# Kernel tuning notes

Hardware: AMD Instinct MI355X
Metric: run time of the kernel (lower is better)

The kernel has to match this reference:

```python
import jax, jax.numpy as jnp
import numpy as np
import math

EMBED_DIM = 256
NUM_HEADS = 8
HEAD_DIM = EMBED_DIM // NUM_HEADS


def rope(t):
    # t: (B, h, S, d). Standard rotate-half RoPE over sequence positions.
    B, h, S, d = t.shape
    half = d // 2
    inv_freq = 1.0 / (10000.0 ** (jnp.arange(0, half, dtype=jnp.float32) / half))
    ang = jnp.arange(S, dtype=jnp.float32)[:, None] * inv_freq[None, :]  # (S, d/2)
    cos = jnp.concatenate([jnp.cos(ang), jnp.cos(ang)], axis=-1)  # (S, d)
    sin = jnp.concatenate([jnp.sin(ang), jnp.sin(ang)], axis=-1)
    t1, t2 = t[..., :half], t[..., half:]
    rot = jnp.concatenate([-t2, t1], axis=-1)
    return t * cos + rot * sin


def setup_inputs() -> dict:
    key = jax.random.key(0)
    ks = jax.random.split(key, 8)
    B, H, W, C = 2, 64, 48, EMBED_DIM
    s = 1.0 / math.sqrt(C)
    return {
        "x": jax.random.normal(ks[0], (B, H, W, C), dtype=jnp.float32),
        "Wq": jax.random.normal(ks[1], (C, C), dtype=jnp.float32) * s,
        "Wk": jax.random.normal(ks[2], (C, C), dtype=jnp.float32) * s,
        "Wv": jax.random.normal(ks[3], (C, C), dtype=jnp.float32) * s,
        "q_bias": jnp.zeros((C,), dtype=jnp.float32),
        "v_bias": jnp.zeros((C,), dtype=jnp.float32),
        "Wo": jax.random.normal(ks[4], (C, C), dtype=jnp.float32) * s,
        "bo": jnp.zeros((C,), dtype=jnp.float32),
    }


def reference(x, Wq, Wk, Wv, q_bias, v_bias, Wo, bo):
    B, H, W, C = x.shape
    S = H * W
    h, d = NUM_HEADS, HEAD_DIM
    xf = x.reshape(B, S, C)
    # QKV projections (torch F.linear: y = x @ W.T + b)
    q = xf @ Wq.T + q_bias
    k = xf @ Wk.T
    v = xf @ Wv.T + v_bias
    # (B, S, h, d) -> (B, h, S, d)
    q = q.reshape(B, S, h, d).transpose(0, 2, 1, 3)
    k = k.reshape(B, S, h, d).transpose(0, 2, 1, 3)
    v = v.reshape(B, S, h, d).transpose(0, 2, 1, 3)
    q = rope(q)
    k = rope(k)
    scale = 1.0 / math.sqrt(d)
    scores = jnp.einsum('bhsd,bhtd->bhst', q, k) * scale  # (B, h, S, S)
    attn = jax.nn.softmax(scores, axis=-1)
    ctx = jnp.einsum('bhst,bhtd->bhsd', attn, v)  # (B, h, S, d)
    ctx = ctx.transpose(0, 2, 1, 3).reshape(B, S, C)
    return ctx @ Wo.T + bo
```

## Files before the change

### kernel.cpp

```cpp
#include <hip/hip_runtime.h>
#include <math.h>

#define B_   2
#define S_   3072
#define C_   256
#define NH   8
#define HD   32
#define HALF 16
#define NELEM (B_*S_*C_)
#define MLROWS (B_*NH*S_)
#define TABN  (S_*HALF)

typedef __attribute__((ext_vector_type(8))) __bf16 bf16x8;
typedef __attribute__((ext_vector_type(4))) float  f32x4;

__device__ __forceinline__ float dot4(float4 a, float4 b) {
    return a.x*b.x + a.y*b.y + a.z*b.z + a.w*b.w;
}

__device__ __forceinline__ void gload_lds16(const void* g, void* l) {
    __builtin_amdgcn_global_load_lds(
        (const __attribute__((address_space(1))) unsigned int*)g,
        (__attribute__((address_space(3))) unsigned int*)l, 16, 0, 0);
}

__device__ __forceinline__ void bsplit(float x, unsigned short& h, unsigned short& lo) {
    __bf16 hb = (__bf16)x;
    float hf = (float)hb;
    __bf16 lb = (__bf16)(x - hf);
    h  = __builtin_bit_cast(unsigned short, hb);
    lo = __builtin_bit_cast(unsigned short, lb);
}

__global__ __launch_bounds__(256) void fsplit_kernel(const float* __restrict__ src,
        unsigned short* __restrict__ hi, unsigned short* __restrict__ lo)
{
    const size_t i = (size_t)blockIdx.x * 256 + threadIdx.x;
    float4 xv = *(const float4*)&src[i*4];
    ushort4 h, l; unsigned short hh, ll;
    bsplit(xv.x, hh, ll); h.x = hh; l.x = ll;
    bsplit(xv.y, hh, ll); h.y = hh; l.y = ll;
    bsplit(xv.z, hh, ll); h.z = hh; l.z = ll;
    bsplit(xv.w, hh, ll); h.w = hh; l.w = ll;
    *(ushort4*)&hi[i*4] = h;
    *(ushort4*)&lo[i*4] = l;
}

__global__ __launch_bounds__(256) void wsplit_kernel(
        const float* __restrict__ Wq, const float* __restrict__ Wk,
        const float* __restrict__ Wv, const float* __restrict__ Wo,
        unsigned short* __restrict__ wqh, unsigned short* __restrict__ wql,
        unsigned short* __restrict__ wkh, unsigned short* __restrict__ wkl,
        unsigned short* __restrict__ wvh, unsigned short* __restrict__ wvl,
        unsigned short* __restrict__ woh, unsigned short* __restrict__ wol)
{
    const float* src; unsigned short *h, *l;
    if      (blockIdx.y == 0) { src = Wq; h = wqh; l = wql; }
    else if (blockIdx.y == 1) { src = Wk; h = wkh; l = wkl; }
    else if (blockIdx.y == 2) { src = Wv; h = wvh; l = wvl; }
    else                      { src = Wo; h = woh; l = wol; }
    const size_t i = (size_t)blockIdx.x * 256 + threadIdx.x;
    float4 xv = *(const float4*)&src[i*4];
    ushort4 hv, lv; unsigned short hh, ll;
    bsplit(xv.x, hh, ll); hv.x = hh; lv.x = ll;
    bsplit(xv.y, hh, ll); hv.y = hh; lv.y = ll;
    bsplit(xv.z, hh, ll); hv.z = hh; lv.z = ll;
    bsplit(xv.w, hh, ll); hv.w = hh; lv.w = ll;
    *(ushort4*)&h[i*4] = hv;
    *(ushort4*)&l[i*4] = lv;
}

__device__ __forceinline__ void gemm_mfma_body(
        const unsigned short* __restrict__ Ahi, const unsigned short* __restrict__ Alo,
        const unsigned short* __restrict__ Whi, const unsigned short* __restrict__ Wlo,
        const float* __restrict__ bias, float* __restrict__ out, float scl)
{
    const int tid = threadIdx.x;
    const int cq  = tid & 15;
    const int gq  = tid >> 4;
    const int m0  = blockIdx.x * 32;
    const int n0  = blockIdx.y * 32;

    const size_t a0 = (size_t)(m0 + cq)      * C_ + gq*8;
    const size_t a1 = (size_t)(m0 + 16 + cq) * C_ + gq*8;
    const size_t w0 = (size_t)(n0 + cq)      * C_ + gq*8;
    const size_t w1 = (size_t)(n0 + 16 + cq) * C_ + gq*8;

    f32x4 acc00 = {0,0,0,0}, acc01 = {0,0,0,0};
    f32x4 acc10 = {0,0,0,0}, acc11 = {0,0,0,0};

    #pragma unroll
    for (int kk = 0; kk < 8; ++kk) {
        const int ko = kk * 32;
        const bf16x8 wh0 = *(const bf16x8*)(Whi + w0 + ko);
        const bf16x8 wh1 = *(const bf16x8*)(Whi + w1 + ko);
        const bf16x8 wl0 = *(const bf16x8*)(Wlo + w0 + ko);
        const bf16x8 wl1 = *(const bf16x8*)(Wlo + w1 + ko);
        const bf16x8 ah0 = *(const bf16x8*)(Ahi + a0 + ko);
        const bf16x8 ah1 = *(const bf16x8*)(Ahi + a1 + ko);
        const bf16x8 al0 = *(const bf16x8*)(Alo + a0 + ko);
        const bf16x8 al1 = *(const bf16x8*)(Alo + a1 + ko);
        acc00 = __builtin_amdgcn_mfma_f32_16x16x32_bf16(wh0, ah0, acc00, 0, 0, 0);
        acc01 = __builtin_amdgcn_mfma_f32_16x16x32_bf16(wh0, ah1, acc01, 0, 0, 0);
        acc10 = __builtin_amdgcn_mfma_f32_16x16x32_bf16(wh1, ah0, acc10, 0, 0, 0);
        acc11 = __builtin_amdgcn_mfma_f32_16x16x32_bf16(wh1, ah1, acc11, 0, 0, 0);
        acc00 = __builtin_amdgcn_mfma_f32_16x16x32_bf16(wh0, al0, acc00, 0, 0, 0);
        acc01 = __builtin_amdgcn_mfma_f32_16x16x32_bf16(wh0, al1, acc01, 0, 0, 0);
        acc10 = __builtin_amdgcn_mfma_f32_16x16x32_bf16(wh1, al0, acc10, 0, 0, 0);
        acc11 = __builtin_amdgcn_mfma_f32_16x16x32_bf16(wh1, al1, acc11, 0, 0, 0);
        acc00 = __builtin_amdgcn_mfma_f32_16x16x32_bf16(wl0, ah0, acc00, 0, 0, 0);
        acc01 = __builtin_amdgcn_mfma_f32_16x16x32_bf16(wl0, ah1, acc01, 0, 0, 0);
        acc10 = __builtin_amdgcn_mfma_f32_16x16x32_bf16(wl1, ah0, acc10, 0, 0, 0);
        acc11 = __builtin_amdgcn_mfma_f32_16x16x32_bf16(wl1, ah1, acc11, 0, 0, 0);
    }

    float4 bv0 = make_float4(0.f, 0.f, 0.f, 0.f);
    float4 bv1 = make_float4(0.f, 0.f, 0.f, 0.f);
    if (bias) {
        bv0 = *(const float4*)&bias[n0 + 4*gq];
        bv1 = *(const float4*)&bias[n0 + 16 + 4*gq];
    }
    float4 o;
    o = make_float4((acc00[0]+bv0.x)*scl, (acc00[1]+bv0.y)*scl,
                    (acc00[2]+bv0.z)*scl, (acc00[3]+bv0.w)*scl);
    *(float4*)&out[(size_t)(m0 + cq)*C_ + n0 + 4*gq] = o;
    o = make_float4((acc01[0]+bv0.x)*scl, (acc01[1]+bv0.y)*scl,
                    (acc01[2]+bv0.z)*scl, (acc01[3]+bv0.w)*scl);
    *(float4*)&out[(size_t)(m0 + 16 + cq)*C_ + n0 + 4*gq] = o;
    o = make_float4((acc10[0]+bv1.x)*scl, (acc10[1]+bv1.y)*scl,
                    (acc10[2]+bv1.z)*scl, (acc10[3]+bv1.w)*scl);
    *(float4*)&out[(size_t)(m0 + cq)*C_ + n0 + 16 + 4*gq] = o;
    o = make_float4((acc11[0]+bv1.x)*scl, (acc11[1]+bv1.y)*scl,
                    (acc11[2]+bv1.z)*scl, (acc11[3]+bv1.w)*scl);
    *(float4*)&out[(size_t)(m0 + 16 + cq)*C_ + n0 + 16 + 4*gq] = o;
}

__global__ __launch_bounds__(64) void qkv_mfma_kernel(
        const unsigned short* __restrict__ xhi, const unsigned short* __restrict__ xlo,
        const unsigned short* __restrict__ wqh, const unsigned short* __restrict__ wql,
        const unsigned short* __restrict__ wkh, const unsigned short* __restrict__ wkl,
        const unsigned short* __restrict__ wvh, const unsigned short* __restrict__ wvl,
        const float* __restrict__ qb, const float* __restrict__ vb,
        float* __restrict__ q, float* __restrict__ k, float* __restrict__ v)
{
    if (blockIdx.z == 0)
        gemm_mfma_body(xhi, xlo, wqh, wql, qb, q, 0.17677669529663687f);
    else if (blockIdx.z == 1)
        gemm_mfma_body(xhi, xlo, wkh, wkl, nullptr, k, 1.0f);
    else
        gemm_mfma_body(xhi, xlo, wvh, wvl, vb, v, 1.0f);
}

__global__ __launch_bounds__(64) void out_gemm_mfma_kernel(
        const unsigned short* __restrict__ chi, const unsigned short* __restrict__ clo,
        const unsigned short* __restrict__ woh, const unsigned short* __restrict__ wol,
        const float* __restrict__ bo, float* __restrict__ out)
{
    gemm_mfma_body(chi, clo, woh, wol, bo, out, 1.0f);
}

__device__ __forceinline__ void gemm_nt_body(const float* __restrict__ A,
                                             const float* __restrict__ W,
                                             const float* __restrict__ bias,
                                             float* __restrict__ out,
                                             float scl)
{
    __shared__ float As[2][64*32];
    __shared__ float Ws[2][64*32];

    const int tid  = threadIdx.x;
    const int wv   = tid >> 6;
    const int tx4  = (tid & 15) * 4;
    const int ty4  = (tid >> 4) * 4;
    const int row0 = blockIdx.x * 64;
    const int col0 = blockIdx.y * 64;

    const int d0  = tid, d1 = tid + 256;
    const int r0s = d0 >> 3, r1s = d1 >> 3;
    const int c0s = (d0 & 7) ^ ((r0s >> 2) & 7);
    const int c1s = (d1 & 7) ^ ((r1s >> 2) & 7);
    const float* a0p = A + (size_t)(row0 + r0s)*C_ + c0s*4;
    const float* a1p = A + (size_t)(row0 + r1s)*C_ + c1s*4;
    const float* w0p = W + (size_t)(col0 + r0s)*C_ + c0s*4;
    const float* w1p = W + (size_t)(col0 + r1s)*C_ + c1s*4;
    const int dst = wv * 256;

#define GSTAGE(kc, buf) { \
        gload_lds16(a0p + (kc), &As[buf][dst]);        \
        gload_lds16(a1p + (kc), &As[buf][dst + 1024]); \
        gload_lds16(w0p + (kc), &Ws[buf][dst]);        \
        gload_lds16(w1p + (kc), &Ws[buf][dst + 1024]); }

    float acc[4][4] = {};
    const int xa = ((tid >> 4) & 7) * 4;
    const int xw = (tid & 7) * 4;

    GSTAGE(0, 0);
    __syncthreads();

    for (int kk = 0; kk < 8; ++kk) {
        const int buf = kk & 1;
        if (kk + 1 < 8) GSTAGE((kk + 1) * 32, buf ^ 1);

        const float* Ab = &As[buf][ty4 * 32];
        const float* Wb = &Ws[buf][tx4 * 32];
        #pragma unroll
        for (int p = 0; p < 8; ++p) {
            const int oa = (p * 4) ^ xa;
            const int ow = (p * 4) ^ xw;
            float4 a0 = *(const float4*)&Ab[oa];
            float4 a1 = *(const float4*)&Ab[32 + oa];
            float4 a2 = *(const float4*)&Ab[64 + oa];
            float4 a3 = *(const float4*)&Ab[96 + oa];
            float4 w0 = *(const float4*)&Wb[ow];
            float4 w1 = *(const float4*)&Wb[32 + ow];
            float4 w2 = *(const float4*)&Wb[64 + ow];
            float4 w3 = *(const float4*)&Wb[96 + ow];
            acc[0][0] += dot4(a0,w0); acc[0][1] += dot4(a0,w1);
            acc[0][2] += dot4(a0,w2); acc[0][3] += dot4(a0,w3);
            acc[1][0] += dot4(a1,w0); acc[1][1] += dot4(a1,w1);
            acc[1][2] += dot4(a1,w2); acc[1][3] += dot4(a1,w3);
            acc[2][0] += dot4(a2,w0); acc[2][1] += dot4(a2,w1);
            acc[2][2] += dot4(a2,w2); acc[2][3] += dot4(a2,w3);
            acc[3][0] += dot4(a3,w0); acc[3][1] += dot4(a3,w1);
            acc[3][2] += dot4(a3,w2); acc[3][3] += dot4(a3,w3);
        }
        __syncthreads();
    }
#undef GSTAGE

    float4 bv = make_float4(0.f, 0.f, 0.f, 0.f);
    if (bias) bv = *(const float4*)&bias[col0 + tx4];
    #pragma unroll
    for (int rr = 0; rr < 4; ++rr) {
        float4 o = make_float4((acc[rr][0] + bv.x)*scl, (acc[rr][1] + bv.y)*scl,
                               (acc[rr][2] + bv.z)*scl, (acc[rr][3] + bv.w)*scl);
        *(float4*)&out[(size_t)(row0 + ty4 + rr)*C_ + col0 + tx4] = o;
    }
}

__global__ __launch_bounds__(256) void qkv_kernel(
        const float* __restrict__ x,
        const float* __restrict__ Wq, const float* __restrict__ Wk, const float* __restrict__ Wv,
        const float* __restrict__ qb, const float* __restrict__ vb,
        float* __restrict__ q, float* __restrict__ k, float* __restrict__ v)
{
    if      (blockIdx.z == 0) gemm_nt_body(x, Wq, qb,      q, 0.17677669529663687f);
    else if (blockIdx.z == 1) gemm_nt_body(x, Wk, nullptr, k, 1.0f);
    else                      gemm_nt_body(x, Wv, vb,      v, 1.0f);
}

__global__ __launch_bounds__(256) void out_gemm_kernel(
        const float* __restrict__ ctx, const float* __restrict__ Wo,
        const float* __restrict__ bo, float* __restrict__ out)
{
    gemm_nt_body(ctx, Wo, bo, out, 1.0f);
}

__global__ __launch_bounds__(256) void rope_tab_kernel(float2* __restrict__ tbl)
{
    const int idx = blockIdx.x * 256 + threadIdx.x;
    const int j = idx & 15;
    const int s = idx >> 4;
    const double invf = exp(-log(10000.0) * (double)j * (1.0 / 16.0));
    const float  angf = (float)((double)s * invf);
    double sn, cs;
    sincos((double)angf, &sn, &cs);
    tbl[idx] = make_float2((float)cs, (float)sn);
}

template<bool TAB>
__global__ __launch_bounds__(256) void rope_kernel(float* __restrict__ q, float* __restrict__ k,
                                                   const float2* __restrict__ tbl,
                                                   unsigned short* __restrict__ qhi,
                                                   unsigned short* __restrict__ qlo,
                                                   unsigned short* __restrict__ khi,
                                                   unsigned short* __restrict__ klo)
{
    const int idx = blockIdx.x * 256 + threadIdx.x;
    const int per_tensor = B_ * S_ * NH * HALF;
    const bool isq = (idx < per_tensor);
    float* t = isq ? q : k;
    const int i   = isq ? idx : idx - per_tensor;
    const int j   = i & 15;
    const int hh  = (i >> 4) & 7;
    const int row = i >> 7;
    const int s   = (row >= S_) ? (row - S_) : row;

    float c, sf;
    if (TAB) {
        const float2 cs2 = tbl[(s << 4) | j];
        c = cs2.x; sf = cs2.y;
    } else {
        const double invf = exp(-log(10000.0) * (double)j * (1.0 / 16.0));
        const float  angf = (float)((double)s * invf);
        double sn, cd;
        sincos((double)angf, &sn, &cd);
        c = (float)cd; sf = (float)sn;
    }

    const size_t base = (size_t)row * C_ + hh * HD + j;
    const float t1 = t[base];
    const float t2 = t[base + HALF];
    const float o1 = t1 * c - t2 * sf;
    const float o2 = t2 * c + t1 * sf;
    t[base]        = o1;
    t[base + HALF] = o2;

    if (TAB) {
        unsigned short* hi = isq ? qhi : khi;
        unsigned short* lo = isq ? qlo : klo;
        const size_t sb = ((size_t)row * NH + hh) * 32;
        unsigned short h1, l1, h2, l2;
        bsplit(o1, h1, l1);
        bsplit(o2, h2, l2);
        hi[sb + j]      = h1;  lo[sb + j]      = l1;
        hi[sb + j + 16] = h2;  lo[sb + j + 16] = l2;
    }
}

__global__ __launch_bounds__(256) void vsplit_kernel(const float* __restrict__ v,
                                                     unsigned short* __restrict__ vthi,
                                                     unsigned short* __restrict__ vtlo)
{
    __shared__ float T[64][33];
    const int t  = threadIdx.x;
    const int kb = blockIdx.x;
    const int hh = blockIdx.y;
    const int b  = blockIdx.z;
    const size_t rowbase = (size_t)b*S_ + kb*64;

    {
        const int r = t >> 2;
        const int p = t & 3;
        float4 a  = *(const float4*)&v[(rowbase + r)*C_ + hh*32 + p*4];
        float4 b2 = *(const float4*)&v[(rowbase + r)*C_ + hh*32 + 16 + p*4];
        *(float4*)&T[r][p*4]      = a;
        *(float4*)&T[r][16 + p*4] = b2;
    }
    __syncthreads();

    const int d = t >> 3;
    const int j = t & 7;
    const int pa = (j & 1)*16 + ((j & 2) ? 4 : 0);
    const int pb = pa + 8;
    ushort4 ha, la, hb, lb;
    unsigned short hs, ls;
    {
        float x0 = T[8*j+0][d], x1 = T[8*j+1][d], x2 = T[8*j+2][d], x3 = T[8*j+3][d];
        bsplit(x0, hs, ls); ha.x = hs; la.x = ls;
        bsplit(x1, hs, ls); ha.y = hs; la.y = ls;
        bsplit(x2, hs, ls); ha.z = hs; la.z = ls;
        bsplit(x3, hs, ls); ha.w = hs; la.w = ls;
        float y0 = T[8*j+4][d], y1 = T[8*j+5][d], y2 = T[8*j+6][d], y3 = T[8*j+7][d];
        bsplit(y0, hs, ls); hb.x = hs; lb.x = ls;
        bsplit(y1, hs, ls); hb.y = hs; lb.y = ls;
        bsplit(y2, hs, ls); hb.z = hs; lb.z = ls;
        bsplit(y3, hs, ls); hb.w = hs; lb.w = ls;
    }
    const size_t ob = (((size_t)b*NH + hh)*32 + d)*S_ + (size_t)(kb*2 + (j >> 2))*32;
    *(ushort4*)&vthi[ob + pa] = ha;
    *(ushort4*)&vthi[ob + pb] = hb;
    *(ushort4*)&vtlo[ob + pa] = la;
    *(ushort4*)&vtlo[ob + pb] = lb;
}

template<int NSPLIT>
__global__ __launch_bounds__(64) void attn_mfma(
        const unsigned short* __restrict__ qhi, const unsigned short* __restrict__ qlo,
        const unsigned short* __restrict__ khi, const unsigned short* __restrict__ klo,
        const unsigned short* __restrict__ vthi, const unsigned short* __restrict__ vtlo,
        float* __restrict__ outp, float* __restrict__ pm, float* __restrict__ pl)
{
    __shared__ unsigned short KH[1024];
    __shared__ unsigned short KL[1024];
    __shared__ unsigned short VTH[2][1024];
    __shared__ unsigned short VTL[2][1024];

    const int tid = threadIdx.x;
    const int cq  = tid & 15;
    const int gq  = tid >> 4;
    const int qb  = blockIdx.x * 32;
    const int hh  = blockIdx.y;
    const int split = blockIdx.z % NSPLIT;
    const int b     = blockIdx.z / NSPLIT;
    const int kt0   = split * (S_ / NSPLIT);
    const int NT    = (S_ / NSPLIT) / 32;

    const size_t rowbase = (size_t)b * S_;
    const int coloff = hh * HD;

    const int sd = tid >> 2;
    const int sp = tid & 3;
    const int ss = sp ^ ((sd >> 1) & 3);

    const unsigned short* kh0 = khi + ((rowbase + kt0 + sd)*NH + hh)*32 + ss*8;
    const unsigned short* kl0 = klo + ((rowbase + kt0 + sd)*NH + hh)*32 + ss*8;
    const size_t vrow_a = (((size_t)b*NH + hh)*32 + sd)      * S_ + kt0;
    const size_t vrow_b = (((size_t)b*NH + hh)*32 + sd + 16) * S_ + kt0;
    const unsigned short* vh_a = vthi + vrow_a + ss*8;
    const unsigned short* vh_b = vthi + vrow_b + ss*8;
    const unsigned short* vl_a = vtlo + vrow_a + ss*8;
    const unsigned short* vl_b = vtlo + vrow_b + ss*8;

#define ISSUE_TILE(t_, vb_) { \
        const size_t ko = (size_t)(t_)*(32*NH*32); \
        const size_t vo = (size_t)(t_)*32; \
        gload_lds16(kh0 + ko,            &KH[0]);   \
        gload_lds16(kh0 + ko + 16*NH*32, &KH[512]); \
        gload_lds16(kl0 + ko,            &KL[0]);   \
        gload_lds16(kl0 + ko + 16*NH*32, &KL[512]); \
        gload_lds16(vh_a + vo, &VTH[vb_][0]);   \
        gload_lds16(vh_b + vo, &VTH[vb_][512]); \
        gload_lds16(vl_a + vo, &VTL[vb_][0]);   \
        gload_lds16(vl_b + vo, &VTL[vb_][512]); }

    ISSUE_TILE(0, 0);

    const size_t q0off = ((rowbase + qb +      cq)*NH + hh)*32 + gq*8;
    const size_t q1off = ((rowbase + qb + 16 + cq)*NH + hh)*32 + gq*8;
    const bf16x8 q0h = *(const bf16x8*)(qhi + q0off);
    const bf16x8 q0l = *(const bf16x8*)(qlo + q0off);
    const bf16x8 q1h = *(const bf16x8*)(qhi + q1off);
    const bf16x8 q1l = *(const bf16x8*)(qlo + q1off);

    const int slot = gq ^ ((cq >> 1) & 3);
    const int fo   = cq*32 + slot*8;

    float m = -1e30f;
    float l0 = 0.f, l1 = 0.f;
    f32x4 acc00 = {0,0,0,0}, acc01 = {0,0,0,0};
    f32x4 acc10 = {0,0,0,0}, acc11 = {0,0,0,0};

    for (int t = 0; t < NT; ++t) {
        const int cur = t & 1;
        asm volatile("s_waitcnt vmcnt(0)" ::: "memory");
        __builtin_amdgcn_sched_barrier(0);

        const bf16x8 kh0f = *(const bf16x8*)&KH[fo];
        const bf16x8 kh1f = *(const bf16x8*)&KH[512 + fo];
        const bf16x8 kl0f = *(const bf16x8*)&KL[fo];
        const bf16x8 kl1f = *(const bf16x8*)&KL[512 + fo];
        asm volatile("s_waitcnt lgkmcnt(0)" ::: "memory");
        __builtin_amdgcn_sched_barrier(0);
        if (t + 1 < NT) ISSUE_TILE(t + 1, cur ^ 1);

        __builtin_amdgcn_s_setprio(1);
        f32x4 s00 = {0,0,0,0}, s01 = {0,0,0,0}, s10 = {0,0,0,0}, s11 = {0,0,0,0};
        s00 = __builtin_amdgcn_mfma_f32_16x16x32_bf16(kh0f, q0h, s00, 0, 0, 0);
        s01 = __builtin_amdgcn_mfma_f32_16x16x32_bf16(kh1f, q0h, s01, 0, 0, 0);
        s10 = __builtin_amdgcn_mfma_f32_16x16x32_bf16(kh0f, q1h, s10, 0, 0, 0);
        s11 = __builtin_amdgcn_mfma_f32_16x16x32_bf16(kh1f, q1h, s11, 0, 0, 0);
        s00 = __builtin_amdgcn_mfma_f32_16x16x32_bf16(kh0f, q0l, s00, 0, 0, 0);
        s01 = __builtin_amdgcn_mfma_f32_16x16x32_bf16(kh1f, q0l, s01, 0, 0, 0);
        s10 = __builtin_amdgcn_mfma_f32_16x16x32_bf16(kh0f, q1l, s10, 0, 0, 0);
        s11 = __builtin_amdgcn_mfma_f32_16x16x32_bf16(kh1f, q1l, s11, 0, 0, 0);
        s00 = __builtin_amdgcn_mfma_f32_16x16x32_bf16(kl0f, q0h, s00, 0, 0, 0);
        s01 = __builtin_amdgcn_mfma_f32_16x16x32_bf16(kl1f, q0h, s01, 0, 0, 0);
        s10 = __builtin_amdgcn_mfma_f32_16x16x32_bf16(kl0f, q1h, s10, 0, 0, 0);
        s11 = __builtin_amdgcn_mfma_f32_16x16x32_bf16(kl1f, q1h, s11, 0, 0, 0);

        float lmax;
        {
            float a = fmaxf(fmaxf(s00[0], s00[1]), fmaxf(s00[2], s00[3]));
            float b2 = fmaxf(fmaxf(s01[0], s01[1]), fmaxf(s01[2], s01[3]));
            float c2 = fmaxf(fmaxf(s10[0], s10[1]), fmaxf(s10[2], s10[3]));
            float d2 = fmaxf(fmaxf(s11[0], s11[1]), fmaxf(s11[2], s11[3]));
            lmax = fmaxf(fmaxf(a, b2), fmaxf(c2, d2));
        }
        if (!__all(lmax - m <= 8.f)) {
            float wm = lmax;
            wm = fmaxf(wm, __shfl_xor(wm, 1));  wm = fmaxf(wm, __shfl_xor(wm, 2));
            wm = fmaxf(wm, __shfl_xor(wm, 4));  wm = fmaxf(wm, __shfl_xor(wm, 8));
            wm = fmaxf(wm, __shfl_xor(wm, 16)); wm = fmaxf(wm, __shfl_xor(wm, 32));
            const float mn = fmaxf(m, wm);
            const float f = __expf(m - mn);
            m = mn; l0 *= f; l1 *= f;
            #pragma unroll
            for (int e = 0; e < 4; ++e) {
                acc00[e] *= f; acc01[e] *= f; acc10[e] *= f; acc11[e] *= f;
            }
        }
        float p00[4], p01[4], p10[4], p11[4];
        #pragma unroll
        for (int e = 0; e < 4; ++e) {
            p00[e] = __expf(s00[e] - m);
            p01[e] = __expf(s01[e] - m);
            p10[e] = __expf(s10[e] - m);
            p11[e] = __expf(s11[e] - m);
        }
        l0 += ((p00[0]+p00[1]) + (p00[2]+p00[3])) + ((p01[0]+p01[1]) + (p01[2]+p01[3]));
        l1 += ((p10[0]+p10[1]) + (p10[2]+p10[3])) + ((p11[0]+p11[1]) + (p11[2]+p11[3]));

        bf16x8 pah0, pal0, pah1, pal1;
        #pragma unroll
        for (int e = 0; e < 4; ++e) {
            __bf16 h;
            h = (__bf16)p00[e]; pah0[e]   = h; pal0[e]   = (__bf16)(p00[e] - (float)h);
            h = (__bf16)p01[e]; pah0[e+4] = h; pal0[e+4] = (__bf16)(p01[e] - (float)h);
            h = (__bf16)p10[e]; pah1[e]   = h; pal1[e]   = (__bf16)(p10[e] - (float)h);
            h = (__bf16)p11[e]; pah1[e+4] = h; pal1[e+4] = (__bf16)(p11[e] - (float)h);
        }

        const bf16x8 vh0 = *(const bf16x8*)&VTH[cur][fo];
        const bf16x8 vh1 = *(const bf16x8*)&VTH[cur][512 + fo];
        const bf16x8 vl0 = *(const bf16x8*)&VTL[cur][fo];
        const bf16x8 vl1 = *(const bf16x8*)&VTL[cur][512 + fo];

        acc00 = __builtin_amdgcn_mfma_f32_16x16x32_bf16(pah0, vh0, acc00, 0, 0, 0);
        acc01 = __builtin_amdgcn_mfma_f32_16x16x32_bf16(pah0, vh1, acc01, 0, 0, 0);
        acc10 = __builtin_amdgcn_mfma_f32_16x16x32_bf16(pah1, vh0, acc10, 0, 0, 0);
        acc11 = __builtin_amdgcn_mfma_f32_16x16x32_bf16(pah1, vh1, acc11, 0, 0, 0);
        acc00 = __builtin_amdgcn_mfma_f32_16x16x32_bf16(pah0, vl0, acc00, 0, 0, 0);
        acc01 = __builtin_amdgcn_mfma_f32_16x16x32_bf16(pah0, vl1, acc01, 0, 0, 0);
        acc10 = __builtin_amdgcn_mfma_f32_16x16x32_bf16(pah1, vl0, acc10, 0, 0, 0);
        acc11 = __builtin_amdgcn_mfma_f32_16x16x32_bf16(pah1, vl1, acc11, 0, 0, 0);
        acc00 = __builtin_amdgcn_mfma_f32_16x16x32_bf16(pal0, vh0, acc00, 0, 0, 0);
        acc01 = __builtin_amdgcn_mfma_f32_16x16x32_bf16(pal0, vh1, acc01, 0, 0, 0);
        acc10 = __builtin_amdgcn_mfma_f32_16x16x32_bf16(pal1, vh0, acc10, 0, 0, 0);
        acc11 = __builtin_amdgcn_mfma_f32_16x16x32_bf16(pal1, vh1, acc11, 0, 0, 0);
        __builtin_amdgcn_s_setprio(0);
    }
#undef ISSUE_TILE

    l0 += __shfl_xor(l0, 16); l0 += __shfl_xor(l0, 32);
    l1 += __shfl_xor(l1, 16); l1 += __shfl_xor(l1, 32);

    float lq0[4], lq1[4];
    #pragma unroll
    for (int r = 0; r < 4; ++r) {
        lq0[r] = __shfl(l0, 4*gq + r);
        lq1[r] = __shfl(l1, 4*gq + r);
    }

    float* obase = (NSPLIT == 1) ? outp : (outp + (size_t)split * NELEM);
    #pragma unroll
    for (int r = 0; r < 4; ++r) {
        const int qrow = qb + 4*gq + r;
        const float i0 = (NSPLIT == 1) ? 1.f / lq0[r] : 1.f;
        const float i1 = (NSPLIT == 1) ? 1.f / lq1[r] : 1.f;
        obase[(rowbase + qrow)*C_ + coloff + cq]           = acc00[r]*i0;
        obase[(rowbase + qrow)*C_ + coloff + 16 + cq]      = acc01[r]*i0;
        obase[(rowbase + qrow + 16)*C_ + coloff + cq]      = acc10[r]*i1;
        obase[(rowbase + qrow + 16)*C_ + coloff + 16 + cq] = acc11[r]*i1;
    }

    if (NSPLIT > 1 && gq == 0) {
        const size_t mlb = (size_t)split*MLROWS + ((size_t)b*NH + hh)*S_;
        pm[mlb + qb + cq]      = m;  pl[mlb + qb + cq]      = l0;
        pm[mlb + qb + 16 + cq] = m;  pl[mlb + qb + 16 + cq] = l1;
    }
}

__global__ __launch_bounds__(64) void attn_fp32(
        const float* __restrict__ q, const float* __restrict__ k,
        const float* __restrict__ v, float* __restrict__ outp)
{
    __shared__ float SM[2][2][16*32];

    const int tid  = threadIdx.x;
    const int sub  = tid & 3;
    const int g    = tid >> 2;
    const int qb   = blockIdx.x * 32;
    const int hh   = blockIdx.y;
    const int b    = blockIdx.z;
    const int NT   = S_ / 16;

    const size_t rowbase = (size_t)b * S_;
    const int coloff = hh * HD;

    const int srow  = tid >> 3;
    const int sxcol = (((tid & 7) ^ (srow & 3)) << 2);
    const float* kstage = &k[(rowbase + srow)*C_ + coloff + sxcol];
    const float* vstage = &v[(rowbase + srow)*C_ + coloff + sxcol];

    const int r0 = qb + g, r1 = qb + g + 16;

#define ISSUE_TILE(t_, bufi) { \
        const float* gk = kstage + (size_t)(t_)*(16*C_); \
        const float* gv = vstage + (size_t)(t_)*(16*C_); \
        float* lk = &SM[bufi][0][0]; \
        float* lv = &SM[bufi][1][0]; \
        gload_lds16(gk        , lk      ); \
        gload_lds16(gk +  8*C_, lk + 256); \
        gload_lds16(gv        , lv      ); \
        gload_lds16(gv +  8*C_, lv + 256); }

    ISSUE_TILE(0, 0);

    float q0[32], q1[32];
    #pragma unroll
    for (int k4 = 0; k4 < 32; k4 += 4) {
        float4 t0 = *(const float4*)&q[(rowbase + r0)*C_ + coloff + k4];
        float4 t1 = *(const float4*)&q[(rowbase + r1)*C_ + coloff + k4];
        q0[k4+0]=t0.x; q0[k4+1]=t0.y; q0[k4+2]=t0.z; q0[k4+3]=t0.w;
        q1[k4+0]=t1.x; q1[k4+1]=t1.y; q1[k4+2]=t1.z; q1[k4+3]=t1.w;
    }

    float m0 = -1e30f, m1 = -1e30f, l0 = 0.f, l1 = 0.f;
    float a0[32] = {}, a1[32] = {};

    for (int t = 0; t < NT; ++t) {
        const int cur = t & 1;
        if (t + 1 < NT) {
            ISSUE_TILE(t + 1, cur ^ 1);
            asm volatile("s_waitcnt vmcnt(4)" ::: "memory");
        } else {
            asm volatile("s_waitcnt vmcnt(0)" ::: "memory");
        }
        __builtin_amdgcn_sched_barrier(0);

        const float* Kc = &SM[cur][0][0];
        const float* Vc = &SM[cur][1][0];

        float s0_[4], s1_[4];
        #pragma unroll
        for (int i = 0; i < 4; ++i) {
            const float* kr = Kc + (sub + 4*i)*32;
            float d0 = 0.f, d1 = 0.f;
            #pragma unroll
            for (int c4 = 0; c4 < 8; ++c4) {
                float4 kk = *(const float4*)&kr[(c4 ^ sub) << 2];
                d0 += q0[c4*4+0]*kk.x + q0[c4*4+1]*kk.y + q0[c4*4+2]*kk.z + q0[c4*4+3]*kk.w;
                d1 += q1[c4*4+0]*kk.x + q1[c4*4+1]*kk.y + q1[c4*4+2]*kk.z + q1[c4*4+3]*kk.w;
            }
            s0_[i] = d0; s1_[i] = d1;
        }
        {
            float tm0 = fmaxf(fmaxf(s0_[0], s0_[1]), fmaxf(s0_[2], s0_[3]));
            float tm1 = fmaxf(fmaxf(s1_[0], s1_[1]), fmaxf(s1_[2], s1_[3]));
            tm0 = fmaxf(tm0, __shfl_xor(tm0, 1)); tm0 = fmaxf(tm0, __shfl_xor(tm0, 2));
            tm1 = fmaxf(tm1, __shfl_xor(tm1, 1)); tm1 = fmaxf(tm1, __shfl_xor(tm1, 2));
            if (!__all((tm0 - m0 <= 8.f) && (tm1 - m1 <= 8.f))) {
                const float mn0 = fmaxf(m0, tm0), mn1 = fmaxf(m1, tm1);
                const float f0 = __expf(m0 - mn0), f1 = __expf(m1 - mn1);
                m0 = mn0; m1 = mn1; l0 *= f0; l1 *= f1;
                #pragma unroll
                for (int d = 0; d < 32; ++d) { a0[d] *= f0; a1[d] *= f1; }
            }
            #pragma unroll
            for (int i = 0; i < 4; ++i) {
                s0_[i] = __expf(s0_[i] - m0);
                s1_[i] = __expf(s1_[i] - m1);
            }
            l0 += (s0_[0] + s0_[1]) + (s0_[2] + s0_[3]);
            l1 += (s1_[0] + s1_[1]) + (s1_[2] + s1_[3]);
        }
        #pragma unroll
        for (int i = 0; i < 4; ++i) {
            const float* vr = Vc + (sub + 4*i)*32;
            const float pj0 = s0_[i], pj1 = s1_[i];
            #pragma unroll
            for (int d4 = 0; d4 < 8; ++d4) {
                float4 vv = *(const float4*)&vr[(d4 ^ sub) << 2];
                a0[d4*4+0] += pj0*vv.x; a0[d4*4+1] += pj0*vv.y;
                a0[d4*4+2] += pj0*vv.z; a0[d4*4+3] += pj0*vv.w;
                a1[d4*4+0] += pj1*vv.x; a1[d4*4+1] += pj1*vv.y;
                a1[d4*4+2] += pj1*vv.z; a1[d4*4+3] += pj1*vv.w;
            }
        }
    }
#undef ISSUE_TILE

    l0 += __shfl_xor(l0, 1); l0 += __shfl_xor(l0, 2);
    l1 += __shfl_xor(l1, 1); l1 += __shfl_xor(l1, 2);
    const float inv0 = 1.f / l0, inv1 = 1.f / l1;
    #pragma unroll
    for (int d = 0; d < 32; ++d) {
        float x0 = a0[d]; x0 += __shfl_xor(x0, 1); x0 += __shfl_xor(x0, 2); a0[d] = x0 * inv0;
        float x1 = a1[d]; x1 += __shfl_xor(x1, 1); x1 += __shfl_xor(x1, 2); a1[d] = x1 * inv1;
    }
    #define WRITE_SLICE(ro, a_, off) { \
        float4 o1 = make_float4(a_[(off)+0],a_[(off)+1],a_[(off)+2],a_[(off)+3]); \
        float4 o2 = make_float4(a_[(off)+4],a_[(off)+5],a_[(off)+6],a_[(off)+7]); \
        *(float4*)&outp[(rowbase + (ro))*C_ + coloff + (off)]     = o1; \
        *(float4*)&outp[(rowbase + (ro))*C_ + coloff + (off) + 4] = o2; }
    if      (sub == 0) { WRITE_SLICE(r0, a0, 0)  WRITE_SLICE(r1, a1, 0)  }
    else if (sub == 1) { WRITE_SLICE(r0, a0, 8)  WRITE_SLICE(r1, a1, 8)  }
    else if (sub == 2) { WRITE_SLICE(r0, a0, 16) WRITE_SLICE(r1, a1, 16) }
    else               { WRITE_SLICE(r0, a0, 24) WRITE_SLICE(r1, a1, 24) }
    #undef WRITE_SLICE
}

template<int NSPLIT>
__global__ __launch_bounds__(256) void combine_split_kernel(
        const float* __restrict__ pacc, const float* __restrict__ pm,
        const float* __restrict__ pl,
        unsigned short* __restrict__ chi, unsigned short* __restrict__ clo)
{
    const int gid = blockIdx.x * 256 + threadIdx.x;
    int rem = gid >> 3;
    const int h = rem & 7; rem >>= 3;
    const int s = rem % S_;
    const int b = rem / S_;

    const size_t i0 = ((size_t)b*NH + h)*S_ + s;
    float mm[NSPLIT], ll[NSPLIT], w[NSPLIT];
    float M = -1e30f;
    #pragma unroll
    for (int i = 0; i < NSPLIT; ++i) {
        mm[i] = pm[i0 + (size_t)i*MLROWS];
        ll[i] = pl[i0 + (size_t)i*MLROWS];
        M = fmaxf(M, mm[i]);
    }
    float L = 0.f;
    #pragma unroll
    for (int i = 0; i < NSPLIT; ++i) { w[i] = __expf(mm[i] - M); L += ll[i]*w[i]; }
    const float invL = 1.f / L;

    const size_t a = (size_t)gid * 4;
    float4 o = make_float4(0.f, 0.f, 0.f, 0.f);
    #pragma unroll
    for (int i = 0; i < NSPLIT; ++i) {
        const float4 x = *(const float4*)&pacc[a + (size_t)i*NELEM];
        o.x += x.x*w[i]; o.y += x.y*w[i]; o.z += x.z*w[i]; o.w += x.w*w[i];
    }
    o.x *= invL; o.y *= invL; o.z *= invL; o.w *= invL;
    ushort4 hv, lv; unsigned short hh, ll2;
    bsplit(o.x, hh, ll2); hv.x = hh; lv.x = ll2;
    bsplit(o.y, hh, ll2); hv.y = hh; lv.y = ll2;
    bsplit(o.z, hh, ll2); hv.z = hh; lv.z = ll2;
    bsplit(o.w, hh, ll2); hv.w = hh; lv.w = ll2;
    *(ushort4*)&chi[a] = hv;
    *(ushort4*)&clo[a] = lv;
}

extern "C" void kernel_launch(void* const* d_in, const int* in_sizes, int n_in,
                              void* d_out, int out_size, void* d_ws, size_t ws_size,
                              hipStream_t stream)
{
    const float* x  = (const float*)d_in[0];
    const float* Wq = (const float*)d_in[1];
    const float* Wk = (const float*)d_in[2];
    const float* Wv = (const float*)d_in[3];
    const float* qb = (const float*)d_in[4];
    const float* vb = (const float*)d_in[5];
    const float* Wo = (const float*)d_in[6];
    const float* bo = (const float*)d_in[7];
    float* out = (float*)d_out;

    float* ws   = (float*)d_ws;
    float* q    = ws;
    float* k    = q + NELEM;
    float* v    = k + NELEM;
    float* ctx  = v + NELEM;
    float* tblf = ctx + NELEM;
    float* pacc = tblf + 2*TABN;
    float* pm   = pacc + (size_t)2*NELEM;
    float* pl   = pm + (size_t)2*MLROWS;
    unsigned short* qhi  = (unsigned short*)(pl + (size_t)2*MLROWS);
    unsigned short* qlo  = qhi + (size_t)NELEM;
    unsigned short* khi  = qlo + (size_t)NELEM;
    unsigned short* klo  = khi + (size_t)NELEM;
    unsigned short* vthi = klo + (size_t)NELEM;
    unsigned short* vtlo = vthi + (size_t)NELEM;

    unsigned short* xhi = (unsigned short*)pacc;
    unsigned short* xlo = xhi + (size_t)NELEM;
    unsigned short* wqh = xlo + (size_t)NELEM;
    unsigned short* wql = wqh + 65536;
    unsigned short* wkh = wql + 65536;
    unsigned short* wkl = wkh + 65536;
    unsigned short* wvh = wkl + 65536;
    unsigned short* wvl = wvh + 65536;
    unsigned short* woh = (unsigned short*)ctx;
    unsigned short* wol = woh + 65536;
    unsigned short* chi = qhi;
    unsigned short* clo = qlo;

    const size_t need = ((size_t)9*NELEM + 2*TABN + 4*MLROWS) * sizeof(float);

    if (ws_size >= need) {
        float2* tbl = (float2*)tblf;
        fsplit_kernel<<<NELEM/1024, 256, 0, stream>>>(x, xhi, xlo);
        wsplit_kernel<<<dim3(64, 4), 256, 0, stream>>>(Wq, Wk, Wv, Wo,
                wqh, wql, wkh, wkl, wvh, wvl, woh, wol);
        qkv_mfma_kernel<<<dim3((B_*S_)/32, C_/32, 3), 64, 0, stream>>>(
                xhi, xlo, wqh, wql, wkh, wkl, wvh, wvl, qb, vb, q, k, v);
        rope_tab_kernel<<<TABN/256, 256, 0, stream>>>(tbl);
        rope_kernel<true><<<6144, 256, 0, stream>>>(q, k, tbl, qhi, qlo, khi, klo);
        vsplit_kernel<<<dim3(S_/64, NH, B_), 256, 0, stream>>>(v, vthi, vtlo);
        attn_mfma<2><<<dim3(S_/32, NH, B_*2), 64, 0, stream>>>(
            qhi, qlo, khi, klo, vthi, vtlo, pacc, pm, pl);
        combine_split_kernel<2><<<(B_*S_*NH*8)/256, 256, 0, stream>>>(
            pacc, pm, pl, chi, clo);
        out_gemm_mfma_kernel<<<dim3((B_*S_)/32, C_/32), 64, 0, stream>>>(
            chi, clo, woh, wol, bo, out);
    } else {
        qkv_kernel<<<dim3(96, 4, 3), 256, 0, stream>>>(x, Wq, Wk, Wv, qb, vb, q, k, v);
        rope_kernel<false><<<6144, 256, 0, stream>>>(q, k, nullptr,
                                                     nullptr, nullptr, nullptr, nullptr);
        attn_fp32<<<dim3(S_/32, NH, B_), 64, 0, stream>>>(q, k, v, ctx);
        out_gemm_kernel<<<dim3(96, 4, 1), 256, 0, stream>>>(ctx, Wo, bo, out);
    }
}
```

Before: 172.8 us.

## Fuse prep kernels and load attention K/V tiles directly into registers

```diff
diff --git a/kernel.cpp b/kernel.cpp
--- a/kernel.cpp
+++ b/kernel.cpp
@@ -32,42 +32,56 @@
     lo = __builtin_bit_cast(unsigned short, lb);
 }
 
-__global__ __launch_bounds__(256) void fsplit_kernel(const float* __restrict__ src,
-        unsigned short* __restrict__ hi, unsigned short* __restrict__ lo)
-{
-    const size_t i = (size_t)blockIdx.x * 256 + threadIdx.x;
-    float4 xv = *(const float4*)&src[i*4];
-    ushort4 h, l; unsigned short hh, ll;
-    bsplit(xv.x, hh, ll); h.x = hh; l.x = ll;
-    bsplit(xv.y, hh, ll); h.y = hh; l.y = ll;
-    bsplit(xv.z, hh, ll); h.z = hh; l.z = ll;
-    bsplit(xv.w, hh, ll); h.w = hh; l.w = ll;
-    *(ushort4*)&hi[i*4] = h;
-    *(ushort4*)&lo[i*4] = l;
-}
-
-__global__ __launch_bounds__(256) void wsplit_kernel(
+__global__ __launch_bounds__(256) void prep_kernel(
+        const float* __restrict__ x,
         const float* __restrict__ Wq, const float* __restrict__ Wk,
         const float* __restrict__ Wv, const float* __restrict__ Wo,
+        unsigned short* __restrict__ xhi, unsigned short* __restrict__ xlo,
         unsigned short* __restrict__ wqh, unsigned short* __restrict__ wql,
         unsigned short* __restrict__ wkh, unsigned short* __restrict__ wkl,
         unsigned short* __restrict__ wvh, unsigned short* __restrict__ wvl,
-        unsigned short* __restrict__ woh, unsigned short* __restrict__ wol)
-{
-    const float* src; unsigned short *h, *l;
-    if      (blockIdx.y == 0) { src = Wq; h = wqh; l = wql; }
-    else if (blockIdx.y == 1) { src = Wk; h = wkh; l = wkl; }
-    else if (blockIdx.y == 2) { src = Wv; h = wvh; l = wvl; }
-    else                      { src = Wo; h = woh; l = wol; }
-    const size_t i = (size_t)blockIdx.x * 256 + threadIdx.x;
-    float4 xv = *(const float4*)&src[i*4];
-    ushort4 hv, lv; unsigned short hh, ll;
-    bsplit(xv.x, hh, ll); hv.x = hh; lv.x = ll;
-    bsplit(xv.y, hh, ll); hv.y = hh; lv.y = ll;
-    bsplit(xv.z, hh, ll); hv.z = hh; lv.z = ll;
-    bsplit(xv.w, hh, ll); hv.w = hh; lv.w = ll;
-    *(ushort4*)&h[i*4] = hv;
-    *(ushort4*)&l[i*4] = lv;
+        unsigned short* __restrict__ woh, unsigned short* __restrict__ wol,
+        float2* __restrict__ tbl)
+{
+    const int bx = blockIdx.x;
+    const int tid = threadIdx.x;
+    if (bx < 1536) {
+        const size_t i = (size_t)bx * 256 + tid;
+        float4 xv = *(const float4*)&x[i*4];
+        ushort4 h, l; unsigned short hh, ll;
+        bsplit(xv.x, hh, ll); h.x = hh; l.x = ll;
+        bsplit(xv.y, hh, ll); h.y = hh; l.y = ll;
+        bsplit(xv.z, hh, ll); h.z = hh; l.z = ll;
+        bsplit(xv.w, hh, ll); h.w = hh; l.w = ll;
+        *(ushort4*)&xhi[i*4] = h;
+        *(ushort4*)&xlo[i*4] = l;
+    } else if (bx < 1792) {
+        const int wb  = bx - 1536;
+        const int mat = wb >> 6;
+        const float* src; unsigned short *h, *l;
+        if      (mat == 0) { src = Wq; h = wqh; l = wql; }
+        else if (mat == 1) { src = Wk; h = wkh; l = wkl; }
+        else if (mat == 2) { src = Wv; h = wvh; l = wvl; }
+        else               { src = Wo; h = woh; l = wol; }
+        const size_t i = (size_t)(wb & 63) * 256 + tid;
+        float4 xv = *(const float4*)&src[i*4];
+        ushort4 hv, lv; unsigned short hh, ll;
+        bsplit(xv.x, hh, ll); hv.x = hh; lv.x = ll;
+        bsplit(xv.y, hh, ll); hv.y = hh; lv.y = ll;
+        bsplit(xv.z, hh, ll); hv.z = hh; lv.z = ll;
+        bsplit(xv.w, hh, ll); hv.w = hh; lv.w = ll;
+        *(ushort4*)&h[i*4] = hv;
+        *(ushort4*)&l[i*4] = lv;
+    } else {
+        const int idx = (bx - 1792) * 256 + tid;
+        const int j = idx & 15;
+        const int s = idx >> 4;
+        const double invf = exp(-log(10000.0) * (double)j * (1.0 / 16.0));
+        const float  angf = (float)((double)s * invf);
+        double sn, cs;
+        sincos((double)angf, &sn, &cs);
+        tbl[idx] = make_float2((float)cs, (float)sn);
+    }
 }
 
 __device__ __forceinline__ void gemm_mfma_body(
@@ -257,18 +271,6 @@
     gemm_nt_body(ctx, Wo, bo, out, 1.0f);
 }
 
-__global__ __launch_bounds__(256) void rope_tab_kernel(float2* __restrict__ tbl)
-{
-    const int idx = blockIdx.x * 256 + threadIdx.x;
-    const int j = idx & 15;
-    const int s = idx >> 4;
-    const double invf = exp(-log(10000.0) * (double)j * (1.0 / 16.0));
-    const float  angf = (float)((double)s * invf);
-    double sn, cs;
-    sincos((double)angf, &sn, &cs);
-    tbl[idx] = make_float2((float)cs, (float)sn);
-}
-
 template<bool TAB>
 __global__ __launch_bounds__(256) void rope_kernel(float* __restrict__ q, float* __restrict__ k,
                                                    const float2* __restrict__ tbl,
@@ -372,11 +374,6 @@
         const unsigned short* __restrict__ vthi, const unsigned short* __restrict__ vtlo,
         float* __restrict__ outp, float* __restrict__ pm, float* __restrict__ pl)
 {
-    __shared__ unsigned short KH[1024];
-    __shared__ unsigned short KL[1024];
-    __shared__ unsigned short VTH[2][1024];
-    __shared__ unsigned short VTL[2][1024];
-
     const int tid = threadIdx.x;
     const int cq  = tid & 15;
     const int gq  = tid >> 4;
@@ -390,32 +387,20 @@
     const size_t rowbase = (size_t)b * S_;
     const int coloff = hh * HD;
 
-    const int sd = tid >> 2;
-    const int sp = tid & 3;
-    const int ss = sp ^ ((sd >> 1) & 3);
-
-    const unsigned short* kh0 = khi + ((rowbase + kt0 + sd)*NH + hh)*32 + ss*8;
-    const unsigned short* kl0 = klo + ((rowbase + kt0 + sd)*NH + hh)*32 + ss*8;
-    const size_t vrow_a = (((size_t)b*NH + hh)*32 + sd)      * S_ + kt0;
-    const size_t vrow_b = (((size_t)b*NH + hh)*32 + sd + 16) * S_ + kt0;
-    const unsigned short* vh_a = vthi + vrow_a + ss*8;
-    const unsigned short* vh_b = vthi + vrow_b + ss*8;
-    const unsigned short* vl_a = vtlo + vrow_a + ss*8;
-    const unsigned short* vl_b = vtlo + vrow_b + ss*8;
-
-#define ISSUE_TILE(t_, vb_) { \
-        const size_t ko = (size_t)(t_)*(32*NH*32); \
-        const size_t vo = (size_t)(t_)*32; \
-        gload_lds16(kh0 + ko,            &KH[0]);   \
-        gload_lds16(kh0 + ko + 16*NH*32, &KH[512]); \
-        gload_lds16(kl0 + ko,            &KL[0]);   \
-        gload_lds16(kl0 + ko + 16*NH*32, &KL[512]); \
-        gload_lds16(vh_a + vo, &VTH[vb_][0]);   \
-        gload_lds16(vh_b + vo, &VTH[vb_][512]); \
-        gload_lds16(vl_a + vo, &VTL[vb_][0]);   \
-        gload_lds16(vl_b + vo, &VTL[vb_][512]); }
-
-    ISSUE_TILE(0, 0);
+    const int KADV = 32*NH*32;
+    const unsigned short* kh_p = khi + ((rowbase + kt0 + cq)*NH + hh)*32 + gq*8;
+    const unsigned short* kl_p = klo + ((rowbase + kt0 + cq)*NH + hh)*32 + gq*8;
+    const size_t vr0 = (((size_t)b*NH + hh)*32 + cq)      * S_ + kt0 + gq*8;
+    const size_t vr1 = (((size_t)b*NH + hh)*32 + 16 + cq) * S_ + kt0 + gq*8;
+    const unsigned short* vh0_p = vthi + vr0;
+    const unsigned short* vh1_p = vthi + vr1;
+    const unsigned short* vl0_p = vtlo + vr0;
+    const unsigned short* vl1_p = vtlo + vr1;
+
+    bf16x8 ckh0 = *(const bf16x8*)(kh_p);
+    bf16x8 ckh1 = *(const bf16x8*)(kh_p + 16*NH*32);
+    bf16x8 ckl0 = *(const bf16x8*)(kl_p);
+    bf16x8 ckl1 = *(const bf16x8*)(kl_p + 16*NH*32);
 
     const size_t q0off = ((rowbase + qb +      cq)*NH + hh)*32 + gq*8;
     const size_t q1off = ((rowbase + qb + 16 + cq)*NH + hh)*32 + gq*8;
@@ -424,41 +409,40 @@
     const bf16x8 q1h = *(const bf16x8*)(qhi + q1off);
     const bf16x8 q1l = *(const bf16x8*)(qlo + q1off);
 
-    const int slot = gq ^ ((cq >> 1) & 3);
-    const int fo   = cq*32 + slot*8;
-
     float m = -1e30f;
     float l0 = 0.f, l1 = 0.f;
     f32x4 acc00 = {0,0,0,0}, acc01 = {0,0,0,0};
     f32x4 acc10 = {0,0,0,0}, acc11 = {0,0,0,0};
 
     for (int t = 0; t < NT; ++t) {
-        const int cur = t & 1;
-        asm volatile("s_waitcnt vmcnt(0)" ::: "memory");
-        __builtin_amdgcn_sched_barrier(0);
-
-        const bf16x8 kh0f = *(const bf16x8*)&KH[fo];
-        const bf16x8 kh1f = *(const bf16x8*)&KH[512 + fo];
-        const bf16x8 kl0f = *(const bf16x8*)&KL[fo];
-        const bf16x8 kl1f = *(const bf16x8*)&KL[512 + fo];
-        asm volatile("s_waitcnt lgkmcnt(0)" ::: "memory");
-        __builtin_amdgcn_sched_barrier(0);
-        if (t + 1 < NT) ISSUE_TILE(t + 1, cur ^ 1);
-
         __builtin_amdgcn_s_setprio(1);
         f32x4 s00 = {0,0,0,0}, s01 = {0,0,0,0}, s10 = {0,0,0,0}, s11 = {0,0,0,0};
-        s00 = __builtin_amdgcn_mfma_f32_16x16x32_bf16(kh0f, q0h, s00, 0, 0, 0);
-        s01 = __builtin_amdgcn_mfma_f32_16x16x32_bf16(kh1f, q0h, s01, 0, 0, 0);
-        s10 = __builtin_amdgcn_mfma_f32_16x16x32_bf16(kh0f, q1h, s10, 0, 0, 0);
-        s11 = __builtin_amdgcn_mfma_f32_16x16x32_bf16(kh1f, q1h, s11, 0, 0, 0);
-        s00 = __builtin_amdgcn_mfma_f32_16x16x32_bf16(kh0f, q0l, s00, 0, 0, 0);
-        s01 = __builtin_amdgcn_mfma_f32_16x16x32_bf16(kh1f, q0l, s01, 0, 0, 0);
-        s10 = __builtin_amdgcn_mfma_f32_16x16x32_bf16(kh0f, q1l, s10, 0, 0, 0);
-        s11 = __builtin_amdgcn_mfma_f32_16x16x32_bf16(kh1f, q1l, s11, 0, 0, 0);
-        s00 = __builtin_amdgcn_mfma_f32_16x16x32_bf16(kl0f, q0h, s00, 0, 0, 0);
-        s01 = __builtin_amdgcn_mfma_f32_16x16x32_bf16(kl1f, q0h, s01, 0, 0, 0);
-        s10 = __builtin_amdgcn_mfma_f32_16x16x32_bf16(kl0f, q1h, s10, 0, 0, 0);
-        s11 = __builtin_amdgcn_mfma_f32_16x16x32_bf16(kl1f, q1h, s11, 0, 0, 0);
+        s00 = __builtin_amdgcn_mfma_f32_16x16x32_bf16(ckh0, q0h, s00, 0, 0, 0);
+        s01 = __builtin_amdgcn_mfma_f32_16x16x32_bf16(ckh1, q0h, s01, 0, 0, 0);
+        s10 = __builtin_amdgcn_mfma_f32_16x16x32_bf16(ckh0, q1h, s10, 0, 0, 0);
+        s11 = __builtin_amdgcn_mfma_f32_16x16x32_bf16(ckh1, q1h, s11, 0, 0, 0);
+        s00 = __builtin_amdgcn_mfma_f32_16x16x32_bf16(ckh0, q0l, s00, 0, 0, 0);
+        s01 = __builtin_amdgcn_mfma_f32_16x16x32_bf16(ckh1, q0l, s01, 0, 0, 0);
+        s10 = __builtin_amdgcn_mfma_f32_16x16x32_bf16(ckh0, q1l, s10, 0, 0, 0);
+        s11 = __builtin_amdgcn_mfma_f32_16x16x32_bf16(ckh1, q1l, s11, 0, 0, 0);
+        s00 = __builtin_amdgcn_mfma_f32_16x16x32_bf16(ckl0, q0h, s00, 0, 0, 0);
+        s01 = __builtin_amdgcn_mfma_f32_16x16x32_bf16(ckl1, q0h, s01, 0, 0, 0);
+        s10 = __builtin_amdgcn_mfma_f32_16x16x32_bf16(ckl0, q1h, s10, 0, 0, 0);
+        s11 = __builtin_amdgcn_mfma_f32_16x16x32_bf16(ckl1, q1h, s11, 0, 0, 0);
+        __builtin_amdgcn_s_setprio(0);
+
+        const int vo = t * 32;
+        const bf16x8 vh0 = *(const bf16x8*)(vh0_p + vo);
+        const bf16x8 vh1 = *(const bf16x8*)(vh1_p + vo);
+        const bf16x8 vl0 = *(const bf16x8*)(vl0_p + vo);
+        const bf16x8 vl1 = *(const bf16x8*)(vl1_p + vo);
+        if (t + 1 < NT) {
+            const size_t ko = (size_t)(t + 1) * KADV;
+            ckh0 = *(const bf16x8*)(kh_p + ko);
+            ckh1 = *(const bf16x8*)(kh_p + ko + 16*NH*32);
+            ckl0 = *(const bf16x8*)(kl_p + ko);
+            ckl1 = *(const bf16x8*)(kl_p + ko + 16*NH*32);
+        }
 
         float lmax;
         {
@@ -502,11 +486,7 @@
             h = (__bf16)p11[e]; pah1[e+4] = h; pal1[e+4] = (__bf16)(p11[e] - (float)h);
         }
 
-        const bf16x8 vh0 = *(const bf16x8*)&VTH[cur][fo];
-        const bf16x8 vh1 = *(const bf16x8*)&VTH[cur][512 + fo];
-        const bf16x8 vl0 = *(const bf16x8*)&VTL[cur][fo];
-        const bf16x8 vl1 = *(const bf16x8*)&VTL[cur][512 + fo];
-
+        __builtin_amdgcn_s_setprio(1);
         acc00 = __builtin_amdgcn_mfma_f32_16x16x32_bf16(pah0, vh0, acc00, 0, 0, 0);
         acc01 = __builtin_amdgcn_mfma_f32_16x16x32_bf16(pah0, vh1, acc01, 0, 0, 0);
         acc10 = __builtin_amdgcn_mfma_f32_16x16x32_bf16(pah1, vh0, acc10, 0, 0, 0);
@@ -521,7 +501,6 @@
         acc11 = __builtin_amdgcn_mfma_f32_16x16x32_bf16(pal1, vh1, acc11, 0, 0, 0);
         __builtin_amdgcn_s_setprio(0);
     }
-#undef ISSUE_TILE
 
     l0 += __shfl_xor(l0, 16); l0 += __shfl_xor(l0, 32);
     l1 += __shfl_xor(l1, 16); l1 += __shfl_xor(l1, 32);
@@ -772,12 +751,10 @@
 
     if (ws_size >= need) {
         float2* tbl = (float2*)tblf;
-        fsplit_kernel<<<NELEM/1024, 256, 0, stream>>>(x, xhi, xlo);
-        wsplit_kernel<<<dim3(64, 4), 256, 0, stream>>>(Wq, Wk, Wv, Wo,
-                wqh, wql, wkh, wkl, wvh, wvl, woh, wol);
+        prep_kernel<<<1984, 256, 0, stream>>>(x, Wq, Wk, Wv, Wo,
+                xhi, xlo, wqh, wql, wkh, wkl, wvh, wvl, woh, wol, tbl);
         qkv_mfma_kernel<<<dim3((B_*S_)/32, C_/32, 3), 64, 0, stream>>>(
                 xhi, xlo, wqh, wql, wkh, wkl, wvh, wvl, qb, vb, q, k, v);
-        rope_tab_kernel<<<TABN/256, 256, 0, stream>>>(tbl);
         rope_kernel<true><<<6144, 256, 0, stream>>>(q, k, tbl, qhi, qlo, khi, klo);
         vsplit_kernel<<<dim3(S_/64, NH, B_), 256, 0, stream>>>(v, vthi, vtlo);
         attn_mfma<2><<<dim3(S_/32, NH, B_*2), 64, 0, stream>>>(
```

Result: slower. 208.2 us (+20.5%).
